# Performance work log

Hardware: AMD Instinct MI355X
Metric: run time of the kernel (lower is better)

## Reference

```python
import jax, jax.numpy as jnp
import numpy as np

N_NODES = 100000
N_EDGES = 1600000
IN_FEATS = 256
HEADS = 4
OUT_FEATS = 32
NEG_SLOPE = 0.2


def setup_inputs() -> dict:
    key = jax.random.key(0)
    k = jax.random.split(key, 7)
    feat = jax.random.normal(k[0], (N_NODES, IN_FEATS), dtype=jnp.float32)
    src = jax.random.randint(k[1], (N_EDGES,), 0, N_NODES)
    dst = jax.random.randint(k[2], (N_EDGES,), 0, N_NODES)
    W = jax.random.normal(k[3], (HEADS * OUT_FEATS, IN_FEATS), dtype=jnp.float32) * 0.05
    attn_l = jax.random.normal(k[4], (1, HEADS, OUT_FEATS), dtype=jnp.float32) * 0.1
    attn_r = jax.random.normal(k[5], (1, HEADS, OUT_FEATS), dtype=jnp.float32) * 0.1
    bias = jnp.zeros((HEADS * OUT_FEATS,), dtype=jnp.float32)
    return {"feat": feat, "src": src, "dst": dst, "W": W,
            "attn_l": attn_l, "attn_r": attn_r, "bias": bias}


def reference(feat, src, dst, W, attn_l, attn_r, bias):
    N = feat.shape[0]
    H, F = attn_l.shape[1], attn_l.shape[2]
    # linear projection: [N, H*F] -> [N, H, F]
    ft = (feat @ W.T).reshape(N, H, F)
    # per-node attention scores [N, H]
    el = jnp.sum(ft * attn_l, axis=-1)
    er = jnp.sum(ft * attn_r, axis=-1)
    # edge scores: u_add_v + LeakyReLU, [E, H]
    e = el[src] + er[dst]
    e = jnp.where(e >= 0, e, NEG_SLOPE * e)
    # edge softmax segmented by destination node
    emax = jax.ops.segment_max(e, dst, num_segments=N)  # [N, H]
    emax = jnp.where(jnp.isfinite(emax), emax, 0.0)
    ex = jnp.exp(e - emax[dst])  # [E, H]
    esum = jax.ops.segment_sum(ex, dst, num_segments=N)  # [N, H]
    a = ex / jnp.maximum(esum[dst], 1e-16)  # [E, H]
    # weighted scatter-sum aggregation: u_mul_e + sum
    msg = ft[src] * a[:, :, None]  # [E, H, F]
    rst = jax.ops.segment_sum(msg, dst, num_segments=N)  # [N, H, F]
    rst = rst + bias.reshape(1, H, F)
    return rst


if __name__ == "__main__":
    out = reference(**setup_inputs())
    print(out.shape, out.dtype)
```

## Files before the change

### kernel.cpp

```cpp
#include <hip/hip_runtime.h>

#define NEG_SLOPE 0.2f
#define G_SHIFT 8
#define G_SIZE  256
#define NB1     256

typedef __attribute__((ext_vector_type(8))) short short8;
typedef __attribute__((ext_vector_type(4))) float floatx4;

__device__ inline unsigned short f32_to_bf16(float f) {
    union { float f; unsigned int u; } c; c.f = f;
    unsigned int u = c.u;
    u += 0x7FFFu + ((u >> 16) & 1u);
    return (unsigned short)(u >> 16);
}
__device__ inline float bf16_lo(unsigned int u) {
    union { unsigned int u; float f; } c; c.u = u << 16; return c.f;
}
__device__ inline float bf16_hi(unsigned int u) {
    union { unsigned int u; float f; } c; c.u = u & 0xFFFF0000u; return c.f;
}

__global__ __launch_bounds__(256) void k_wconv(const float* __restrict__ W,
                                               unsigned short* __restrict__ Wb,
                                               int n) {
    int i = blockIdx.x * 256 + threadIdx.x;
    if (i < n) Wb[i] = f32_to_bf16(W[i]);
}

__global__ __launch_bounds__(256) void k_gemm_mfma(const float* __restrict__ feat,
                                                   const unsigned short* __restrict__ Wb,
                                                   unsigned short* __restrict__ ftb,
                                                   int M) {
    const int tid  = threadIdx.x;
    const int wave = tid >> 6;
    const int lane = tid & 63;
    const int l16  = lane & 15;
    const int quad = lane >> 4;
    const int mw   = blockIdx.x * 64 + wave * 16;

    int arow = mw + l16;
    if (arow >= M) arow = M - 1;
    const float* aptr = feat + (size_t)arow * 256 + quad * 8;

    floatx4 acc[8];
#pragma unroll
    for (int t = 0; t < 8; ++t) acc[t] = (floatx4){0.f, 0.f, 0.f, 0.f};

#pragma unroll
    for (int k0 = 0; k0 < 256; k0 += 32) {
        float4 a0 = *(const float4*)(aptr + k0);
        float4 a1 = *(const float4*)(aptr + k0 + 4);
        short8 af;
        af[0] = (short)f32_to_bf16(a0.x);
        af[1] = (short)f32_to_bf16(a0.y);
        af[2] = (short)f32_to_bf16(a0.z);
        af[3] = (short)f32_to_bf16(a0.w);
        af[4] = (short)f32_to_bf16(a1.x);
        af[5] = (short)f32_to_bf16(a1.y);
        af[6] = (short)f32_to_bf16(a1.z);
        af[7] = (short)f32_to_bf16(a1.w);
#pragma unroll
        for (int t = 0; t < 8; ++t) {
            short8 bf = *(const short8*)(Wb + (size_t)(t * 16 + l16) * 256 + k0 + quad * 8);
            acc[t] = __builtin_amdgcn_mfma_f32_16x16x32_bf16(af, bf, acc[t], 0, 0, 0);
        }
    }

#pragma unroll
    for (int t = 0; t < 8; ++t) {
#pragma unroll
        for (int r = 0; r < 4; ++r) {
            int row = mw + quad * 4 + r;
            if (row < M)
                ftb[(size_t)row * 128 + t * 16 + l16] = f32_to_bf16(acc[t][r]);
        }
    }
}

__global__ __launch_bounds__(256) void k_elr(const unsigned short* __restrict__ ftb,
                                             const float* __restrict__ al,
                                             const float* __restrict__ ar,
                                             float* __restrict__ el,
                                             float* __restrict__ er,
                                             int NH) {
    int i = blockIdx.x * 256 + threadIdx.x;
    if (i >= NH) return;
    int h = i & 3;
    const unsigned int* f = (const unsigned int*)ftb + (size_t)i * 16;
    const float* lp = al + h * 32;
    const float* rp = ar + h * 32;
    float sl = 0.f, sr = 0.f;
#pragma unroll
    for (int j = 0; j < 16; ++j) {
        unsigned int u = f[j];
        float f0 = bf16_lo(u), f1 = bf16_hi(u);
        sl += f0 * lp[2 * j] + f1 * lp[2 * j + 1];
        sr += f0 * rp[2 * j] + f1 * rp[2 * j + 1];
    }
    el[i] = sl;
    er[i] = sr;
}

__global__ __launch_bounds__(256) void k_count(const int* __restrict__ dst,
                                               int* __restrict__ counts,
                                               int E, int CH, int B) {
    __shared__ int hist[512];
    int j = blockIdx.x, t = threadIdx.x;
    for (int bk = t; bk < B; bk += 256) hist[bk] = 0;
    __syncthreads();
    int lo = j * CH, hi = min(E, lo + CH);
    for (int i = lo + t; i < hi; i += 256)
        atomicAdd(&hist[dst[i] >> G_SHIFT], 1);
    __syncthreads();
    for (int bk = t; bk < B; bk += 256) counts[bk * NB1 + j] = hist[bk];
}

__global__ __launch_bounds__(256) void k_scan1(const int* __restrict__ deg,
                                               int* __restrict__ offs,
                                               int* __restrict__ bsum, int n) {
    __shared__ int ls[256];
    int b = blockIdx.x, t = threadIdx.x;
    int base = b * 1024 + t * 4;
    int d0 = (base + 0 < n) ? deg[base + 0] : 0;
    int d1 = (base + 1 < n) ? deg[base + 1] : 0;
    int d2 = (base + 2 < n) ? deg[base + 2] : 0;
    int d3 = (base + 3 < n) ? deg[base + 3] : 0;
    int s = d0 + d1 + d2 + d3;
    ls[t] = s;
    __syncthreads();
    for (int o = 1; o < 256; o <<= 1) {
        int v = (t >= o) ? ls[t - o] : 0;
        __syncthreads();
        ls[t] += v;
        __syncthreads();
    }
    int excl = ls[t] - s;
    if (base + 0 < n) offs[base + 0] = excl;
    if (base + 1 < n) offs[base + 1] = excl + d0;
    if (base + 2 < n) offs[base + 2] = excl + d0 + d1;
    if (base + 3 < n) offs[base + 3] = excl + d0 + d1 + d2;
    if (t == 255) bsum[b] = ls[255];
}

__global__ __launch_bounds__(256) void k_scan2(int* __restrict__ bsum, int NB) {
    __shared__ int ls[256];
    int t = threadIdx.x;
    int v = (t < NB) ? bsum[t] : 0;
    ls[t] = v;
    __syncthreads();
    for (int o = 1; o < 256; o <<= 1) {
        int u = (t >= o) ? ls[t - o] : 0;
        __syncthreads();
        ls[t] += u;
        __syncthreads();
    }
    if (t < NB) bsum[t] = ls[t] - v;
}

__global__ __launch_bounds__(256) void k_scan3(int* __restrict__ arr,
                                               const int* __restrict__ bsum,
                                               int n) {
    int i = blockIdx.x * 256 + threadIdx.x;
    if (i < n) arr[i] += bsum[i >> 10];
}

__global__ __launch_bounds__(256) void k_partition(const int* __restrict__ src,
                                                   const int* __restrict__ dst,
                                                   const int* __restrict__ scanned,
                                                   int* __restrict__ part,
                                                   int E, int CH, int B) {
    __shared__ int curs[512];
    int j = blockIdx.x, t = threadIdx.x;
    for (int bk = t; bk < B; bk += 256) curs[bk] = scanned[bk * NB1 + j];
    __syncthreads();
    int lo = j * CH, hi = min(E, lo + CH);
    for (int i = lo + t; i < hi; i += 256) {
        int d = dst[i];
        int bk = d >> G_SHIFT;
        int pos = atomicAdd(&curs[bk], 1);
        if (pos >= 0 && pos < E)
            part[pos] = ((d & (G_SIZE - 1)) << 17) | src[i];
    }
}

__global__ __launch_bounds__(256) void k_bucket(const int* __restrict__ scanned,
                                                const int* __restrict__ part,
                                                int* __restrict__ offs,
                                                int* __restrict__ esrc,
                                                int E, int B, int N) {
    __shared__ int hist[256], ls[256], curs[256];
    int b = blockIdx.x, t = threadIdx.x;
    int start = scanned[b * NB1];
    int end   = (b == B - 1) ? E : scanned[(b + 1) * NB1];

    hist[t] = 0;
    __syncthreads();
    for (int i = start + t; i < end; i += 256)
        atomicAdd(&hist[(part[i] >> 17) & 255], 1);
    __syncthreads();

    int h = hist[t];
    ls[t] = h;
    __syncthreads();
    for (int o = 1; o < 256; o <<= 1) {
        int v = (t >= o) ? ls[t - o] : 0;
        __syncthreads();
        ls[t] += v;
        __syncthreads();
    }
    int excl = ls[t] - h;
    curs[t] = excl;
    int node = b * G_SIZE + t;
    if (node < N) offs[node] = start + excl;
    if (b == B - 1 && t == 0) offs[N] = E;
    __syncthreads();

    for (int i = start + t; i < end; i += 256) {
        int p = part[i];
        int pos = start + atomicAdd(&curs[(p >> 17) & 255], 1);
        if (pos >= 0 && pos < E) esrc[pos] = p & 0x1FFFF;
    }
}

__global__ __launch_bounds__(256) void k_aggr_csr(const int* __restrict__ offs,
                                                  const int* __restrict__ esrc,
                                                  const float* __restrict__ el,
                                                  const float* __restrict__ er,
                                                  const unsigned short* __restrict__ ftb,
                                                  const float* __restrict__ bias,
                                                  float* __restrict__ out,
                                                  int N) {
    int node = blockIdx.x * 4 + (threadIdx.x >> 6);
    if (node >= N) return;
    int lane = threadIdx.x & 63;
    int h = lane >> 4;
    float er_h = er[node * 4 + h];

    int j   = offs[node];
    int end = offs[node + 1];

    float2 acc = make_float2(0.f, 0.f);
    float  wsum = 0.f;
    const unsigned int* ftu = (const unsigned int*)ftb;

    int s_next = (j < end) ? esrc[j] : 0;
    for (; j < end; ++j) {
        int s = s_next;
        if (j + 1 < end) s_next = esrc[j + 1];
        float x = el[s * 4 + h] + er_h;
        x = x >= 0.f ? x : NEG_SLOPE * x;
        float w = __expf(x);
        wsum += w;
        unsigned int u = ftu[(size_t)s * 64 + lane];
        acc.x += w * bf16_lo(u);
        acc.y += w * bf16_hi(u);
    }
    float scale = 1.0f / fmaxf(wsum, 1e-16f);
    float2 bv = ((const float2*)bias)[lane];
    float2 o;
    o.x = acc.x * scale + bv.x;
    o.y = acc.y * scale + bv.y;
    ((float2*)out)[(size_t)node * 64 + lane] = o;
}

__global__ __launch_bounds__(256) void k_init_fb(float* __restrict__ out,
                                                 const float* __restrict__ bias,
                                                 float* __restrict__ esum,
                                                 int n_out, int n_esum) {
    int i = blockIdx.x * 256 + threadIdx.x;
    if (i < n_out)  out[i]  = bias[i & 127];
    if (i < n_esum) esum[i] = 0.0f;
}

__global__ __launch_bounds__(256) void k_esum_fb(const int* __restrict__ src,
                                                 const int* __restrict__ dst,
                                                 const float* __restrict__ el,
                                                 const float* __restrict__ er,
                                                 float* __restrict__ esum,
                                                 int E4) {
    int i = blockIdx.x * 256 + threadIdx.x;
    if (i >= E4) return;
    int e = i >> 2, h = i & 3;
    int s = src[e], d = dst[e];
    float x = el[s * 4 + h] + er[d * 4 + h];
    x = x >= 0.f ? x : NEG_SLOPE * x;
    atomicAdd(&esum[d * 4 + h], __expf(x));
}

__global__ __launch_bounds__(256) void k_aggr_fb(const int* __restrict__ src,
                                                 const int* __restrict__ dst,
                                                 const float* __restrict__ el,
                                                 const float* __restrict__ er,
                                                 const float* __restrict__ esum,
                                                 const unsigned short* __restrict__ ftb,
                                                 float* __restrict__ out,
                                                 int E) {
    int i = blockIdx.x * 256 + threadIdx.x;
    int e = i >> 6;
    if (e >= E) return;
    int c = i & 63;
    int h = c >> 4;
    int s = src[e], d = dst[e];
    float x = el[s * 4 + h] + er[d * 4 + h];
    x = x >= 0.f ? x : NEG_SLOPE * x;
    float a = __expf(x) / fmaxf(esum[d * 4 + h], 1e-16f);
    unsigned int u = ((const unsigned int*)ftb)[(size_t)s * 64 + c];
    float* o = out + (size_t)d * 128 + c * 2;
    atomicAdd(o + 0, bf16_lo(u) * a);
    atomicAdd(o + 1, bf16_hi(u) * a);
}

extern "C" void kernel_launch(void* const* d_in, const int* in_sizes, int n_in,
                              void* d_out, int out_size, void* d_ws, size_t ws_size,
                              hipStream_t stream) {
    const float* feat   = (const float*)d_in[0];
    const int*   src    = (const int*)d_in[1];
    const int*   dst    = (const int*)d_in[2];
    const float* W      = (const float*)d_in[3];
    const float* attn_l = (const float*)d_in[4];
    const float* attn_r = (const float*)d_in[5];
    const float* bias   = (const float*)d_in[6];

    const int N  = in_sizes[0] / 256;
    const int E  = in_sizes[1];
    const int NW = in_sizes[3];
    float* out = (float*)d_out;

    const int B  = (N + G_SIZE - 1) / G_SIZE;
    const int CH = (E + NB1 - 1) / NB1;
    const int n2 = B * NB1;

    unsigned short* ftb = (unsigned short*)d_ws;
    unsigned short* Wb  = ftb + (size_t)N * 128;
    float* el = (float*)(Wb + NW);
    float* er = el + (size_t)N * 4;
    int* offs    = (int*)(er + (size_t)N * 4);
    int* counts  = offs + (N + 1);
    int* scanned = counts + n2;
    int* bsum    = scanned + n2;
    int* part    = bsum + 256;
    int* esrc    = part + E;
    size_t need = (size_t)((char*)(esrc + E) - (char*)d_ws);

    k_wconv<<<(NW + 255) / 256, 256, 0, stream>>>(W, Wb, NW);
    k_gemm_mfma<<<(N + 63) / 64, 256, 0, stream>>>(feat, Wb, ftb, N);
    k_elr<<<(N * 4 + 255) / 256, 256, 0, stream>>>(ftb, attn_l, attn_r, el, er, N * 4);

    if (ws_size >= need) {
        const int NBs = (n2 + 1023) / 1024;
        k_count<<<NB1, 256, 0, stream>>>(dst, counts, E, CH, B);
        k_scan1<<<NBs, 256, 0, stream>>>(counts, scanned, bsum, n2);
        k_scan2<<<1, 256, 0, stream>>>(bsum, NBs);
        k_scan3<<<(n2 + 255) / 256, 256, 0, stream>>>(scanned, bsum, n2);
        k_partition<<<NB1, 256, 0, stream>>>(src, dst, scanned, part, E, CH, B);
        k_bucket<<<B, 256, 0, stream>>>(scanned, part, offs, esrc, E, B, N);
        k_aggr_csr<<<(N + 3) / 4, 256, 0, stream>>>(offs, esrc, el, er, ftb, bias, out, N);
    } else {
        float* esum = (float*)(er + (size_t)N * 4);
        k_init_fb<<<(N * 128 + 255) / 256, 256, 0, stream>>>(out, bias, esum, N * 128, N * 4);
        k_esum_fb<<<(E * 4 + 255) / 256, 256, 0, stream>>>(src, dst, el, er, esum, E * 4);
        k_aggr_fb<<<((size_t)E * 64 + 255) / 256, 256, 0, stream>>>(src, dst, el, er, esum, ftb, out, E);
    }
}
```

Baseline: 406.1 us.

## Batch edge weights across lanes with bpermute and fold scan fixup into consumers

In the CSR aggregation kernel, each wavefront now loads up to 16 edge sources and computes their per-head attention weights in parallel, one edge-head pair per lane. It then broadcasts the weights and sources with ds_bpermute and unrolls the feature gather by two. This removes the serial per-edge load of esrc and el and the exp on the dependent chain, and allows two feature loads in flight at once. Separately, the k_scan3 block-offset fixup kernel is removed and its add is done inline where partition and bucket read the scanned array, which saves one launch and one pass over the array.

```diff
diff --git a/kernel.cpp b/kernel.cpp
--- a/kernel.cpp
+++ b/kernel.cpp
@@ -158,21 +158,18 @@
     if (t < NB) bsum[t] = ls[t] - v;
 }
 
-__global__ __launch_bounds__(256) void k_scan3(int* __restrict__ arr,
-                                               const int* __restrict__ bsum,
-                                               int n) {
-    int i = blockIdx.x * 256 + threadIdx.x;
-    if (i < n) arr[i] += bsum[i >> 10];
-}
-
 __global__ __launch_bounds__(256) void k_partition(const int* __restrict__ src,
                                                    const int* __restrict__ dst,
                                                    const int* __restrict__ scanned,
+                                                   const int* __restrict__ bsum,
                                                    int* __restrict__ part,
                                                    int E, int CH, int B) {
     __shared__ int curs[512];
     int j = blockIdx.x, t = threadIdx.x;
-    for (int bk = t; bk < B; bk += 256) curs[bk] = scanned[bk * NB1 + j];
+    for (int bk = t; bk < B; bk += 256) {
+        int idx = bk * NB1 + j;
+        curs[bk] = scanned[idx] + bsum[idx >> 10];
+    }
     __syncthreads();
     int lo = j * CH, hi = min(E, lo + CH);
     for (int i = lo + t; i < hi; i += 256) {
@@ -185,14 +182,20 @@
 }
 
 __global__ __launch_bounds__(256) void k_bucket(const int* __restrict__ scanned,
+                                                const int* __restrict__ bsum,
                                                 const int* __restrict__ part,
                                                 int* __restrict__ offs,
                                                 int* __restrict__ esrc,
                                                 int E, int B, int N) {
     __shared__ int hist[256], ls[256], curs[256];
     int b = blockIdx.x, t = threadIdx.x;
-    int start = scanned[b * NB1];
-    int end   = (b == B - 1) ? E : scanned[(b + 1) * NB1];
+    int i0 = b * NB1;
+    int start = scanned[i0] + bsum[i0 >> 10];
+    int end = E;
+    if (b < B - 1) {
+        int i1 = (b + 1) * NB1;
+        end = scanned[i1] + bsum[i1 >> 10];
+    }
 
     hist[t] = 0;
     __syncthreads();
@@ -234,27 +237,53 @@
     int node = blockIdx.x * 4 + (threadIdx.x >> 6);
     if (node >= N) return;
     int lane = threadIdx.x & 63;
-    int h = lane >> 4;
-    float er_h = er[node * 4 + h];
-
-    int j   = offs[node];
-    int end = offs[node + 1];
+    int h1 = lane & 3;
+    int h2 = lane >> 4;
+    float er1 = er[node * 4 + h1];
+
+    int start = offs[node];
+    int deg   = offs[node + 1] - start;
 
     float2 acc = make_float2(0.f, 0.f);
     float  wsum = 0.f;
     const unsigned int* ftu = (const unsigned int*)ftb;
-
-    int s_next = (j < end) ? esrc[j] : 0;
-    for (; j < end; ++j) {
-        int s = s_next;
-        if (j + 1 < end) s_next = esrc[j + 1];
-        float x = el[s * 4 + h] + er_h;
-        x = x >= 0.f ? x : NEG_SLOPE * x;
-        float w = __expf(x);
-        wsum += w;
-        unsigned int u = ftu[(size_t)s * 64 + lane];
-        acc.x += w * bf16_lo(u);
-        acc.y += w * bf16_hi(u);
+    const int h2b = h2 << 2;
+
+    int p = 0;
+    while (p < deg) {
+        int cnt = min(16, deg - p);
+        float w = 0.f;
+        int   s = 0;
+        if ((lane >> 2) < cnt) {
+            s = esrc[start + p + (lane >> 2)];
+            float x = el[s * 4 + h1] + er1;
+            x = x >= 0.f ? x : NEG_SLOPE * x;
+            w = __expf(x);
+        }
+        int j = 0;
+        for (; j + 2 <= cnt; j += 2) {
+            int i0 = (j << 4) + h2b;
+            int i1 = i0 + 16;
+            float w0 = __int_as_float(__builtin_amdgcn_ds_bpermute(i0, __float_as_int(w)));
+            int   s0 = __builtin_amdgcn_ds_bpermute(i0, s);
+            float w1 = __int_as_float(__builtin_amdgcn_ds_bpermute(i1, __float_as_int(w)));
+            int   s1 = __builtin_amdgcn_ds_bpermute(i1, s);
+            unsigned int u0 = ftu[(size_t)s0 * 64 + lane];
+            unsigned int u1 = ftu[(size_t)s1 * 64 + lane];
+            wsum += w0 + w1;
+            acc.x += w0 * bf16_lo(u0) + w1 * bf16_lo(u1);
+            acc.y += w0 * bf16_hi(u0) + w1 * bf16_hi(u1);
+        }
+        if (j < cnt) {
+            int i0 = (j << 4) + h2b;
+            float w0 = __int_as_float(__builtin_amdgcn_ds_bpermute(i0, __float_as_int(w)));
+            int   s0 = __builtin_amdgcn_ds_bpermute(i0, s);
+            unsigned int u0 = ftu[(size_t)s0 * 64 + lane];
+            wsum += w0;
+            acc.x += w0 * bf16_lo(u0);
+            acc.y += w0 * bf16_hi(u0);
+        }
+        p += cnt;
     }
     float scale = 1.0f / fmaxf(wsum, 1e-16f);
     float2 bv = ((const float2*)bias)[lane];
@@ -352,9 +381,8 @@
         k_count<<<NB1, 256, 0, stream>>>(dst, counts, E, CH, B);
         k_scan1<<<NBs, 256, 0, stream>>>(counts, scanned, bsum, n2);
         k_scan2<<<1, 256, 0, stream>>>(bsum, NBs);
-        k_scan3<<<(n2 + 255) / 256, 256, 0, stream>>>(scanned, bsum, n2);
-        k_partition<<<NB1, 256, 0, stream>>>(src, dst, scanned, part, E, CH, B);
-        k_bucket<<<B, 256, 0, stream>>>(scanned, part, offs, esrc, E, B, N);
+        k_partition<<<NB1, 256, 0, stream>>>(src, dst, scanned, bsum, part, E, CH, B);
+        k_bucket<<<B, 256, 0, stream>>>(scanned, bsum, part, offs, esrc, E, B, N);
         k_aggr_csr<<<(N + 3) / 4, 256, 0, stream>>>(offs, esrc, el, er, ftb, bias, out, N);
     } else {
         float* esum = (float*)(er + (size_t)N * 4);
```

Result: faster. 374.1 us (-7.9%).
